# Kernel tuning notes

Hardware: AMD Instinct MI355X
Metric: run time of the kernel (lower is better)

The kernel has to match this reference:

```python
import jax, jax.numpy as jnp
import numpy as np

N = 50000      # nodes
E = 800000     # edges (avg degree 16)
F_IN = 128     # num_node_features
D = 64         # embedding_size (= per-head out_channels)
H = 4          # heads
ED = 20        # edge_dim (hardcoded in module)
SLOPE = 0.2    # GATv2 leaky_relu negative slope
N_LAYERS = 3   # conv applied 3 times with shared weights


def setup_inputs() -> dict:
    key = jax.random.key(0)
    ks = jax.random.split(key, 12)
    s = 0.1
    return {
        "x": jax.random.normal(ks[0], (N, F_IN), jnp.float32),
        "edge_attr": jax.random.normal(ks[1], (E, 2), jnp.float32),
        "edge_index": jax.random.randint(ks[2], (2, E), 0, N, dtype=jnp.int32),
        # f: Linear(F_IN, D)
        "f_W": jax.random.normal(ks[3], (F_IN, D), jnp.float32) * s,
        "f_b": jnp.zeros((D,), jnp.float32),
        # fe: Linear(2, ED)
        "fe_W": jax.random.normal(ks[4], (2, ED), jnp.float32) * s,
        "fe_b": jnp.zeros((ED,), jnp.float32),
        # GATv2Conv lin_l / lin_r: Linear(D, H*D)
        "Wl": jax.random.normal(ks[5], (D, H * D), jnp.float32) * s,
        "bl": jnp.zeros((H * D,), jnp.float32),
        "Wr": jax.random.normal(ks[6], (D, H * D), jnp.float32) * s,
        "br": jnp.zeros((H * D,), jnp.float32),
        # lin_edge: Linear(ED, H*D, bias=False)
        "We": jax.random.normal(ks[7], (ED, H * D), jnp.float32) * s,
        # attention vector att: [H, D]
        "att": jax.random.normal(ks[8], (H, D), jnp.float32) * s,
        # final bias (concat=False -> size D)
        "bias": jnp.zeros((D,), jnp.float32),
    }


def _gatv2_conv(h, e_emb, src, dst, Wl, bl, Wr, br, We, att, bias):
    # h: [N, D], e_emb: [E, ED], src/dst: [E]
    xl = (h @ Wl + bl).reshape(-1, H, D)        # source transform  [N,H,D]
    xr = (h @ Wr + br).reshape(-1, H, D)        # target transform  [N,H,D]
    ee = (e_emb @ We).reshape(-1, H, D)         # edge transform    [E,H,D]
    m = jax.nn.leaky_relu(xl[src] + xr[dst] + ee, SLOPE)  # [E,H,D]
    score = jnp.einsum('ehd,hd->eh', m, att)    # [E,H]
    # segment softmax over incoming edges of each dst node
    smax = jax.ops.segment_max(score, dst, num_segments=N)   # [N,H]
    ex = jnp.exp(score - smax[dst])
    denom = jax.ops.segment_sum(ex, dst, num_segments=N)     # [N,H]
    alpha = ex / denom[dst]                                  # [E,H]
    out = jax.ops.segment_sum(alpha[:, :, None] * xl[src], dst, num_segments=N)  # [N,H,D]
    return out.mean(axis=1) + bias              # concat=False -> head mean, [N,D]


def reference(x, edge_attr, edge_index, f_W, f_b, fe_W, fe_b, Wl, bl, Wr, br, We, att, bias):
    src, dst = edge_index[0], edge_index[1]
    h = jax.nn.relu(x @ f_W + f_b)
    e = jax.nn.relu(edge_attr @ fe_W + fe_b)
    for _ in range(N_LAYERS):
        h = jax.nn.relu(_gatv2_conv(h, e, src, dst, Wl, bl, Wr, br, We, att, bias))
    return h
```

## Files before the change

### kernel.cpp

```cpp
#include <hip/hip_runtime.h>
#include <math.h>

typedef float v2f __attribute__((ext_vector_type(2)));

#define LN2_INV 1.4426950408889634f

__device__ __forceinline__ float fexp2(float x) {
#if __has_builtin(__builtin_amdgcn_exp2f)
    return __builtin_amdgcn_exp2f(x);
#else
    return exp2f(x);
#endif
}

__device__ __forceinline__ int rdlane_i(int v, int k) {
    return __builtin_amdgcn_readlane(v, k);
}

__device__ __forceinline__ v2f max2(v2f a, float b) {
    v2f r; r.x = fmaxf(a.x, b); r.y = fmaxf(a.y, b); return r;
}
__device__ __forceinline__ v2f min2(v2f a, float b) {
    v2f r; r.x = fminf(a.x, b); r.y = fminf(a.y, b); return r;
}

#define DPP_ROW_ADD(V, CTRL) \
    V += __int_as_float(__builtin_amdgcn_update_dpp(0, __float_as_int(V), CTRL, 0xf, 0xf, true));

__global__ __launch_bounds__(256) void k_h0(const float* __restrict__ x,
                                            const float* __restrict__ fW,
                                            const float* __restrict__ fb,
                                            float* __restrict__ h0) {
    __shared__ __align__(16) float xs[8 * 128];
    int t = threadIdx.x;
    int base = blockIdx.x * 8;
#pragma unroll
    for (int r = 0; r < 4; ++r) { int j = r * 256 + t; xs[j] = x[base * 128 + j]; }
    __syncthreads();
    int c = t & 63, half = t >> 6;
    float acc0 = fb[c], acc1 = fb[c];
    int m0 = half, m1 = half + 4;
#pragma unroll 8
    for (int k0 = 0; k0 < 128; k0 += 4) {
        float4 a = *(const float4*)&xs[m0 * 128 + k0];
        float4 b = *(const float4*)&xs[m1 * 128 + k0];
        float w0 = fW[(k0 + 0) * 64 + c], w1 = fW[(k0 + 1) * 64 + c];
        float w2 = fW[(k0 + 2) * 64 + c], w3 = fW[(k0 + 3) * 64 + c];
        acc0 = fmaf(a.x, w0, fmaf(a.y, w1, fmaf(a.z, w2, fmaf(a.w, w3, acc0))));
        acc1 = fmaf(b.x, w0, fmaf(b.y, w1, fmaf(b.z, w2, fmaf(b.w, w3, acc1))));
    }
    h0[(base + m0) * 64 + c] = fmaxf(acc0, 0.f);
    h0[(base + m1) * 64 + c] = fmaxf(acc1, 0.f);
}

__global__ __launch_bounds__(256) void k_xlxr(const float* __restrict__ h,
                                              const float* __restrict__ Wl,
                                              const float* __restrict__ Wr,
                                              const float* __restrict__ bl,
                                              const float* __restrict__ br,
                                              float* __restrict__ xl,
                                              float* __restrict__ xr) {
    __shared__ __align__(16) float hs[16 * 64];
    int t = threadIdx.x;
    int base = blockIdx.x * 16;
#pragma unroll
    for (int r = 0; r < 4; ++r) hs[r * 256 + t] = h[base * 64 + r * 256 + t];
    __syncthreads();
    float bL = bl[t], bR = br[t];
    float accl[16], accr[16];
#pragma unroll
    for (int m = 0; m < 16; ++m) { accl[m] = bL; accr[m] = bR; }
#pragma unroll 4
    for (int k0 = 0; k0 < 64; k0 += 4) {
        float wl[4], wr[4];
#pragma unroll
        for (int q = 0; q < 4; ++q) {
            wl[q] = Wl[(k0 + q) * 256 + t];
            wr[q] = Wr[(k0 + q) * 256 + t];
        }
#pragma unroll
        for (int m = 0; m < 16; ++m) {
            float4 hv = *(const float4*)&hs[m * 64 + k0];
            accl[m] = fmaf(hv.x, wl[0], fmaf(hv.y, wl[1], fmaf(hv.z, wl[2], fmaf(hv.w, wl[3], accl[m]))));
            accr[m] = fmaf(hv.x, wr[0], fmaf(hv.y, wr[1], fmaf(hv.z, wr[2], fmaf(hv.w, wr[3], accr[m]))));
        }
    }
#pragma unroll
    for (int m = 0; m < 16; ++m) {
        xl[(base + m) * 256 + t] = accl[m];
        xr[(base + m) * 256 + t] = accr[m];
    }
}

__global__ void k_zero(int* __restrict__ deg, int* __restrict__ counter, int Nn) {
    int i = blockIdx.x * 256 + threadIdx.x;
    if (i < Nn) deg[i] = 0;
    if (i == 0) *counter = 0;
}

__global__ void k_count(const int* __restrict__ dstArr, int* __restrict__ deg, int Ee) {
    int e = blockIdx.x * 256 + threadIdx.x;
    if (e < Ee) atomicAdd(&deg[dstArr[e]], 1);
}

__global__ void k_alloc(const int* __restrict__ deg, int* __restrict__ counter,
                        int* __restrict__ start, int* __restrict__ cursor, int Nn) {
    int n = blockIdx.x * 256 + threadIdx.x;
    if (n < Nn) {
        int d = deg[n];
        int b = atomicAdd(counter, d);
        start[n] = b;
        cursor[n] = b;
    }
}

__global__ void k_fill(const int* __restrict__ dstArr, const int* __restrict__ srcArr,
                       const float* __restrict__ eattr, const float* __restrict__ feW,
                       const float* __restrict__ feb, int* __restrict__ cursor,
                       int* __restrict__ rec, int Ee) {
    int e = blockIdx.x * 256 + threadIdx.x;
    if (e >= Ee) return;
    float a0 = eattr[2 * e], a1 = eattr[2 * e + 1];
    int p = atomicAdd(&cursor[dstArr[e]], 1);
    float* r = (float*)(rec + (size_t)p * 24);
    float s[20];
#pragma unroll
    for (int k = 0; k < 20; ++k)
        s[k] = fmaxf(fmaf(a0, feW[k], fmaf(a1, feW[20 + k], feb[k])), 0.f);
#pragma unroll
    for (int j = 0; j < 5; ++j)
        ((float4*)r)[j] = make_float4(s[4 * j], s[4 * j + 1], s[4 * j + 2], s[4 * j + 3]);
    ((int*)r)[20] = srcArr[e];
}

__global__ __launch_bounds__(256, 3) void k_edge(
    const float4* __restrict__ xl4p, const float4* __restrict__ xr4p,
    const float* __restrict__ att, const float4* __restrict__ We4,
    const int* __restrict__ rec, const int* __restrict__ start,
    const int* __restrict__ deg, const float* __restrict__ bias,
    float* __restrict__ hout, int Nn) {
    const int lane = threadIdx.x & 63;
    const int n = (int)((blockIdx.x * 256u + threadIdx.x) >> 6);
    if (n >= Nn) return;

    const int dn = __builtin_amdgcn_readfirstlane(deg[n]);
    float4 bias4 = ((const float4*)bias)[lane & 15];
    if (dn == 0) {
        if (lane < 16) {
            float4 o = make_float4(fmaxf(bias4.x, 0.f), fmaxf(bias4.y, 0.f),
                                   fmaxf(bias4.z, 0.f), fmaxf(bias4.w, 0.f));
            ((float4*)hout)[(size_t)n * 16 + lane] = o;
        }
        return;
    }
    const int s0 = __builtin_amdgcn_readfirstlane(start[n]);
    const int* rb = rec + (size_t)s0 * 24 + (lane & 31);

    float4 attv = ((const float4*)att)[lane];
    v2f att01 = {attv.x * LN2_INV, attv.y * LN2_INV};
    v2f att23 = {attv.z * LN2_INV, attv.w * LN2_INV};
    v2f at201 = 0.2f * att01, at223 = 0.2f * att23;
    float4 xrv = xr4p[(size_t)n * 64 + lane];
    v2f xr01 = {xrv.x, xrv.y}, xr23 = {xrv.z, xrv.w};
    v2f we01[20], we23[20];
#pragma unroll
    for (int k = 0; k < 20; ++k) {
        float4 w = We4[k * 64 + lane];
        we01[k].x = w.x; we01[k].y = w.y;
        we23[k].x = w.z; we23[k].y = w.w;
    }
    const int bperm = ((lane & 48) | 15) << 2;

    v2f acc01 = {0.f, 0.f}, acc23 = {0.f, 0.f};
    float l = 0.f;

    int i1 = dn > 1 ? 1 : 0;
    int rv0 = rb[0];
    int rv1 = rb[(size_t)i1 * 24];
    int src0 = rdlane_i(rv0, 20);
    float4 xl0 = xl4p[(size_t)src0 * 64 + lane];

    for (int i = 0; i < dn; ++i) {
        int i2 = (i + 2 < dn) ? (i + 2) : (dn - 1);
        int rv2 = rb[(size_t)i2 * 24];
        int src1 = rdlane_i(rv1, 20);
        float4 xl1 = xl4p[(size_t)src1 * 64 + lane];

        v2f xl01 = {xl0.x, xl0.y}, xl23 = {xl0.z, xl0.w};

        v2f ee01, ee23;
        {
            float sk = __int_as_float(rdlane_i(rv0, 0));
            ee01 = sk * we01[0];
            ee23 = sk * we23[0];
        }
#pragma unroll
        for (int k = 1; k < 20; ++k) {
            float sk = __int_as_float(rdlane_i(rv0, k));
            ee01 += sk * we01[k];
            ee23 += sk * we23[k];
        }

        v2f v01 = (xl01 + xr01) + ee01;
        v2f v23 = (xl23 + xr23) + ee23;
        v2f p01 = att01 * max2(v01, 0.f) + at201 * min2(v01, 0.f);
        v2f p23 = att23 * max2(v23, 0.f) + at223 * min2(v23, 0.f);
        v2f pr = p01 + p23;
        float ps = pr.x + pr.y;
        DPP_ROW_ADD(ps, 0x111)
        DPP_ROW_ADD(ps, 0x112)
        DPP_ROW_ADD(ps, 0x114)
        DPP_ROW_ADD(ps, 0x118)
        float sc = __int_as_float(
            __builtin_amdgcn_ds_bpermute(bperm, __float_as_int(ps)));
        float w_ = fexp2(sc);
        l += w_;
        acc01 += w_ * xl01;
        acc23 += w_ * xl23;

        rv0 = rv1; rv1 = rv2; xl0 = xl1;
    }

    float inv = 0.25f / l;
    float4 r = make_float4(acc01.x * inv, acc01.y * inv, acc23.x * inv, acc23.y * inv);
    r.x += __shfl_xor(r.x, 16, 64); r.x += __shfl_xor(r.x, 32, 64);
    r.y += __shfl_xor(r.y, 16, 64); r.y += __shfl_xor(r.y, 32, 64);
    r.z += __shfl_xor(r.z, 16, 64); r.z += __shfl_xor(r.z, 32, 64);
    r.w += __shfl_xor(r.w, 16, 64); r.w += __shfl_xor(r.w, 32, 64);
    if (lane < 16) {
        float4 o = make_float4(fmaxf(r.x + bias4.x, 0.f), fmaxf(r.y + bias4.y, 0.f),
                               fmaxf(r.z + bias4.z, 0.f), fmaxf(r.w + bias4.w, 0.f));
        ((float4*)hout)[(size_t)n * 16 + lane] = o;
    }
}

extern "C" void kernel_launch(void* const* d_in, const int* in_sizes, int n_in,
                              void* d_out, int out_size, void* d_ws, size_t ws_size,
                              hipStream_t stream) {
    const float* x     = (const float*)d_in[0];
    const float* eattr = (const float*)d_in[1];
    const int*   eidx  = (const int*)d_in[2];
    const float* fW    = (const float*)d_in[3];
    const float* fb    = (const float*)d_in[4];
    const float* feW   = (const float*)d_in[5];
    const float* feb   = (const float*)d_in[6];
    const float* Wl    = (const float*)d_in[7];
    const float* bl    = (const float*)d_in[8];
    const float* Wr    = (const float*)d_in[9];
    const float* br    = (const float*)d_in[10];
    const float* We    = (const float*)d_in[11];
    const float* att   = (const float*)d_in[12];
    const float* bias  = (const float*)d_in[13];
    float* out = (float*)d_out;

    const int N = in_sizes[0] / 128;
    const int E = in_sizes[1] / 2;
    const int* srcArr = eidx;
    const int* dstArr = eidx + E;

    char* p = (char*)d_ws;
    auto alloc = [&](size_t bytes) -> char* {
        char* r = p;
        p += (bytes + 255) & ~(size_t)255;
        return r;
    };
    float* hA   = (float*)alloc((size_t)N * 64 * 4);
    float* hB   = (float*)alloc((size_t)N * 64 * 4);
    float* xl   = (float*)alloc((size_t)N * 256 * 4);
    float* xr   = (float*)alloc((size_t)N * 256 * 4);
    int* deg    = (int*)alloc((size_t)N * 4);
    int* start  = (int*)alloc((size_t)N * 4);
    int* cursor = (int*)alloc((size_t)N * 4);
    int* counter = (int*)alloc(256);
    int* rec    = (int*)alloc((size_t)E * 24 * 4);

    k_h0<<<N / 8, 256, 0, stream>>>(x, fW, fb, hA);
    k_zero<<<(N + 255) / 256, 256, 0, stream>>>(deg, counter, N);
    k_count<<<(E + 255) / 256, 256, 0, stream>>>(dstArr, deg, E);
    k_alloc<<<(N + 255) / 256, 256, 0, stream>>>(deg, counter, start, cursor, N);
    k_fill<<<(E + 255) / 256, 256, 0, stream>>>(dstArr, srcArr, eattr, feW, feb,
                                                cursor, rec, E);

    const float* hin = hA;
    for (int layer = 0; layer < 3; ++layer) {
        float* hout = (layer == 2) ? out : ((layer == 0) ? hB : hA);
        k_xlxr<<<N / 16, 256, 0, stream>>>(hin, Wl, Wr, bl, br, xl, xr);
        k_edge<<<(N * 64) / 256, 256, 0, stream>>>(
            (const float4*)xl, (const float4*)xr, att, (const float4*)We,
            rec, start, deg, bias, hout, N);
        hin = hout;
    }
}
```

Before: 919.2 us.

## Reload We per edge and use packed FMA with abs-form leaky ReLU scoring

The edge kernel no longer holds the 20×4 We values in registers across the edge loop. It reloads them from global memory (cache) on every edge iteration, which cuts register pressure and should raise occupancy, at the cost of extra loads per edge. The edge-embedding dot product becomes two independent chains of inline-asm v_pk_fma_f32 with scalar operands. The leaky-ReLU-times-att is rewritten as 0.6·a·v + 0.4·a·|v| so it needs fewer instructions, and the rec buffer gets 256 bytes of padding.

After: 2.025 ms. +120.3%, slower.

```diff
diff --git a/kernel.cpp b/kernel.cpp
--- a/kernel.cpp
+++ b/kernel.cpp
@@ -17,12 +17,10 @@
     return __builtin_amdgcn_readlane(v, k);
 }
 
-__device__ __forceinline__ v2f max2(v2f a, float b) {
-    v2f r; r.x = fmaxf(a.x, b); r.y = fmaxf(a.y, b); return r;
-}
-__device__ __forceinline__ v2f min2(v2f a, float b) {
-    v2f r; r.x = fminf(a.x, b); r.y = fminf(a.y, b); return r;
-}
+#define PKFMA_S(ACC, SK, W) \
+    asm("v_pk_fma_f32 %0, %1, %2, %0" : "+v"(ACC) : "s"(SK), "v"(W));
+#define PKADD(D, A, B) \
+    asm("v_pk_add_f32 %0, %1, %2" : "=v"(D) : "v"(A), "v"(B));
 
 #define DPP_ROW_ADD(V, CTRL) \
     V += __int_as_float(__builtin_amdgcn_update_dpp(0, __float_as_int(V), CTRL, 0xf, 0xf, true));
@@ -157,21 +155,15 @@
     const int* rb = rec + (size_t)s0 * 24 + (lane & 31);
 
     float4 attv = ((const float4*)att)[lane];
-    v2f att01 = {attv.x * LN2_INV, attv.y * LN2_INV};
-    v2f att23 = {attv.z * LN2_INV, attv.w * LN2_INV};
-    v2f at201 = 0.2f * att01, at223 = 0.2f * att23;
+    float4 aA = make_float4(0.6f * LN2_INV * attv.x, 0.6f * LN2_INV * attv.y,
+                            0.6f * LN2_INV * attv.z, 0.6f * LN2_INV * attv.w);
+    float4 aB = make_float4(0.4f * LN2_INV * attv.x, 0.4f * LN2_INV * attv.y,
+                            0.4f * LN2_INV * attv.z, 0.4f * LN2_INV * attv.w);
     float4 xrv = xr4p[(size_t)n * 64 + lane];
     v2f xr01 = {xrv.x, xrv.y}, xr23 = {xrv.z, xrv.w};
-    v2f we01[20], we23[20];
-#pragma unroll
-    for (int k = 0; k < 20; ++k) {
-        float4 w = We4[k * 64 + lane];
-        we01[k].x = w.x; we01[k].y = w.y;
-        we23[k].x = w.z; we23[k].y = w.w;
-    }
     const int bperm = ((lane & 48) | 15) << 2;
 
-    v2f acc01 = {0.f, 0.f}, acc23 = {0.f, 0.f};
+    float acc0 = 0.f, acc1 = 0.f, acc2 = 0.f, acc3 = 0.f;
     float l = 0.f;
 
     int i1 = dn > 1 ? 1 : 0;
@@ -186,43 +178,60 @@
         int src1 = rdlane_i(rv1, 20);
         float4 xl1 = xl4p[(size_t)src1 * 64 + lane];
 
+        v2f eA01 = {0.f, 0.f}, eA23 = {0.f, 0.f};
+        v2f eB01 = {0.f, 0.f}, eB23 = {0.f, 0.f};
+#pragma unroll
+        for (int k = 0; k < 10; ++k) {
+            float4 wa = We4[k * 64 + lane];
+            float4 wb = We4[(k + 10) * 64 + lane];
+            float ska = __int_as_float(rdlane_i(rv0, k));
+            float skb = __int_as_float(rdlane_i(rv0, k + 10));
+            v2f sa = {ska, ska};
+            v2f sb = {skb, skb};
+            v2f wa01 = {wa.x, wa.y}, wa23 = {wa.z, wa.w};
+            v2f wb01 = {wb.x, wb.y}, wb23 = {wb.z, wb.w};
+            PKFMA_S(eA01, sa, wa01)
+            PKFMA_S(eA23, sa, wa23)
+            PKFMA_S(eB01, sb, wb01)
+            PKFMA_S(eB23, sb, wb23)
+        }
+        v2f ee01, ee23;
+        PKADD(ee01, eA01, eB01)
+        PKADD(ee23, eA23, eB23)
+
         v2f xl01 = {xl0.x, xl0.y}, xl23 = {xl0.z, xl0.w};
-
-        v2f ee01, ee23;
-        {
-            float sk = __int_as_float(rdlane_i(rv0, 0));
-            ee01 = sk * we01[0];
-            ee23 = sk * we23[0];
-        }
-#pragma unroll
-        for (int k = 1; k < 20; ++k) {
-            float sk = __int_as_float(rdlane_i(rv0, k));
-            ee01 += sk * we01[k];
-            ee23 += sk * we23[k];
-        }
-
-        v2f v01 = (xl01 + xr01) + ee01;
-        v2f v23 = (xl23 + xr23) + ee23;
-        v2f p01 = att01 * max2(v01, 0.f) + at201 * min2(v01, 0.f);
-        v2f p23 = att23 * max2(v23, 0.f) + at223 * min2(v23, 0.f);
-        v2f pr = p01 + p23;
-        float ps = pr.x + pr.y;
-        DPP_ROW_ADD(ps, 0x111)
-        DPP_ROW_ADD(ps, 0x112)
-        DPP_ROW_ADD(ps, 0x114)
-        DPP_ROW_ADD(ps, 0x118)
+        v2f t01, t23, v01, v23;
+        PKADD(t01, xl01, xr01)
+        PKADD(t23, xl23, xr23)
+        PKADD(v01, t01, ee01)
+        PKADD(v23, t23, ee23)
+
+        float tt = aB.x * __builtin_fabsf(v01.x);
+        tt = fmaf(aA.x, v01.x, tt);
+        tt = fmaf(aB.y, __builtin_fabsf(v01.y), tt);
+        tt = fmaf(aA.y, v01.y, tt);
+        tt = fmaf(aB.z, __builtin_fabsf(v23.x), tt);
+        tt = fmaf(aA.z, v23.x, tt);
+        tt = fmaf(aB.w, __builtin_fabsf(v23.y), tt);
+        tt = fmaf(aA.w, v23.y, tt);
+        DPP_ROW_ADD(tt, 0x111)
+        DPP_ROW_ADD(tt, 0x112)
+        DPP_ROW_ADD(tt, 0x114)
+        DPP_ROW_ADD(tt, 0x118)
         float sc = __int_as_float(
-            __builtin_amdgcn_ds_bpermute(bperm, __float_as_int(ps)));
+            __builtin_amdgcn_ds_bpermute(bperm, __float_as_int(tt)));
         float w_ = fexp2(sc);
         l += w_;
-        acc01 += w_ * xl01;
-        acc23 += w_ * xl23;
+        acc0 = fmaf(w_, xl0.x, acc0);
+        acc1 = fmaf(w_, xl0.y, acc1);
+        acc2 = fmaf(w_, xl0.z, acc2);
+        acc3 = fmaf(w_, xl0.w, acc3);
 
         rv0 = rv1; rv1 = rv2; xl0 = xl1;
     }
 
     float inv = 0.25f / l;
-    float4 r = make_float4(acc01.x * inv, acc01.y * inv, acc23.x * inv, acc23.y * inv);
+    float4 r = make_float4(acc0 * inv, acc1 * inv, acc2 * inv, acc3 * inv);
     r.x += __shfl_xor(r.x, 16, 64); r.x += __shfl_xor(r.x, 32, 64);
     r.y += __shfl_xor(r.y, 16, 64); r.y += __shfl_xor(r.y, 32, 64);
     r.z += __shfl_xor(r.z, 16, 64); r.z += __shfl_xor(r.z, 32, 64);
@@ -272,7 +281,7 @@
     int* start  = (int*)alloc((size_t)N * 4);
     int* cursor = (int*)alloc((size_t)N * 4);
     int* counter = (int*)alloc(256);
-    int* rec    = (int*)alloc((size_t)E * 24 * 4);
+    int* rec    = (int*)alloc((size_t)E * 24 * 4 + 256);
 
     k_h0<<<N / 8, 256, 0, stream>>>(x, fW, fb, hA);
     k_zero<<<(N + 255) / 256, 256, 0, stream>>>(deg, counter, N);
```
